# Kernel optimization log

Hardware: AMD Instinct MI355X
Metric: run time of the kernel (lower is better)

The kernel has to match this reference:

```python
import jax, jax.numpy as jnp
import numpy as np

IN_C = 256
INTER_C = 128  # in_channels // reduction_ratio


def setup_inputs() -> dict:
    key = jax.random.key(0)
    ks = jax.random.split(key, 9)
    s = 1.0 / np.sqrt(IN_C)
    si = 1.0 / np.sqrt(INTER_C)
    return {
        "x": jax.random.normal(ks[0], (8, IN_C, 64, 64), dtype=jnp.float32),
        "g_w": jax.random.uniform(ks[1], (INTER_C, IN_C), jnp.float32, -s, s),
        "g_b": jax.random.uniform(ks[2], (INTER_C,), jnp.float32, -s, s),
        "theta_w": jax.random.uniform(ks[3], (INTER_C, IN_C), jnp.float32, -s, s),
        "theta_b": jax.random.uniform(ks[4], (INTER_C,), jnp.float32, -s, s),
        "phi_w": jax.random.uniform(ks[5], (INTER_C, IN_C), jnp.float32, -s, s),
        "phi_b": jax.random.uniform(ks[6], (INTER_C,), jnp.float32, -s, s),
        "W_w": jax.random.uniform(ks[7], (IN_C, INTER_C), jnp.float32, -si, si),
        "W_b": jax.random.uniform(ks[8], (IN_C,), jnp.float32, -si, si),
    }


def _conv1x1(x, w, b):
    # x: [b, cin, h, w]; w: [cout, cin] -> [b, cout, h, w]
    return jnp.einsum('oc,bchw->bohw', w, x) + b[None, :, None, None]


def reference(x, g_w, g_b, theta_w, theta_b, phi_w, phi_b, W_w, W_b):
    b, c, h, w = x.shape
    n = h * w
    g_x = _conv1x1(x, g_w, g_b).reshape(b, INTER_C, n)        # [b, i, n]
    theta_x = _conv1x1(x, theta_w, theta_b).reshape(b, INTER_C, n)
    phi_x = _conv1x1(x, phi_w, phi_b).reshape(b, INTER_C, n)
    # f[b, q, k] = sum_i theta[b, i, q] * phi[b, i, k]
    f = jnp.einsum('biq,bik->bqk', theta_x, phi_x)            # [b, n, n]
    f_div_C = jax.nn.softmax(f, axis=-1)
    # y[b, q, i] = sum_k f_div_C[b, q, k] * g_x[b, i, k]
    y = jnp.einsum('bqk,bik->biq', f_div_C, g_x)              # [b, i, n]
    y = y.reshape(b, INTER_C, h, w)
    W_y = _conv1x1(y, W_w, W_b)
    return W_y + x
```

## Files before the change

### kernel.cpp

```cpp
#include <hip/hip_runtime.h>
#include <hip/hip_bf16.h>
#include <stdint.h>

#define NB 8
#define CIN 256
#define IC 128
#define NP 4096

typedef __attribute__((ext_vector_type(8))) short s8v;
typedef __attribute__((ext_vector_type(4))) short s4v;
typedef __attribute__((ext_vector_type(16))) float f16v;
typedef __attribute__((ext_vector_type(4))) float f4v;

#define MFMA32(a, b, c) __builtin_amdgcn_mfma_f32_32x32x16_bf16(a, b, c, 0, 0, 0)

__device__ __forceinline__ unsigned short f2bf(float f) {
  union { float f; unsigned int u; } v; v.f = f;
  unsigned int u = v.u;
  return (unsigned short)((u + 0x7FFFu + ((u >> 16) & 1u)) >> 16);
}

__device__ __forceinline__ unsigned short f2bf_h(float f) {
  __hip_bfloat16 h = __float2bfloat16(f);
  union { __hip_bfloat16 h; unsigned short u; } cv; cv.h = h;
  return cv.u;
}

__device__ __forceinline__ float bf2f(short s) {
  union { unsigned int u; float f; } cv;
  cv.u = ((unsigned int)(unsigned short)s) << 16;
  return cv.f;
}

typedef const unsigned int __attribute__((address_space(1))) gas_u32;
typedef unsigned int __attribute__((address_space(3))) las_u32;
__device__ __forceinline__ void gload_lds16(const void* g, void* l) {
  __builtin_amdgcn_global_load_lds((gas_u32*)g, (las_u32*)l, 16, 0, 0);
}

__global__ __launch_bounds__(256) void k_wprep(const float* __restrict__ thw,
    const float* __restrict__ phw, const float* __restrict__ gw,
    const float* __restrict__ Ww, unsigned short* __restrict__ wB) {
  const int g = blockIdx.x >> 5;
  const int base = (blockIdx.x & 31) * 1024 + threadIdx.x * 4;
  const float* src = (g == 0) ? thw : ((g == 1) ? phw : ((g == 2) ? gw : Ww));
  const float sc = (g == 0) ? 1.44269504f : 1.0f;
  const f4v v = *(const f4v*)(src + base);
  ushort4 u;
  u.x = f2bf(v[0] * sc); u.y = f2bf(v[1] * sc);
  u.z = f2bf(v[2] * sc); u.w = f2bf(v[3] * sc);
  *(ushort4*)(wB + g * 32768 + base) = u;
}

__global__ __launch_bounds__(256) void k_conv3(const float* __restrict__ x,
    const unsigned short* __restrict__ wB,
    const float* __restrict__ thb, const float* __restrict__ phb,
    const float* __restrict__ gb,
    unsigned short* __restrict__ Qg, unsigned short* __restrict__ Kg,
    unsigned short* __restrict__ Vtg) {
  __shared__ unsigned short X[64 * 256];
  __shared__ unsigned short T[64][72];
  const int t = threadIdx.x, lane = t & 63, wid = t >> 6;
  const int b = blockIdx.x & 7;
  const int p0 = (blockIdx.x >> 3) * 64;
  const int hl = lane >> 5;
  const float* xb = x + (size_t)b * CIN * NP + p0;
  const int cl = t >> 4;
  const int p4 = (t & 15) * 4;
  for (int sub = 0; sub < 4; ++sub) {
    const int c0 = sub * 64;
#pragma unroll
    for (int j = 0; j < 4; ++j) {
      const int cloc = cl + j * 16;
      const f4v v = *(const f4v*)(xb + (size_t)(c0 + cloc) * NP + p4);
      ushort4 u;
      u.x = f2bf(v[0]); u.y = f2bf(v[1]); u.z = f2bf(v[2]); u.w = f2bf(v[3]);
      *(ushort4*)&T[cloc][p4 ^ ((cloc & 7) * 8)] = u;
    }
    __syncthreads();
    const int p = t >> 2;
#pragma unroll
    for (int half = 0; half < 2; ++half) {
      const int cg = (t & 3) + half * 4;
      alignas(16) unsigned short outv[8];
#pragma unroll
      for (int k = 0; k < 8; ++k)
        outv[k] = T[cg * 8 + k][p ^ (k * 8)];
      const int cc = sub * 8 + cg;
      *(uint4*)&X[p * 256 + 8 * (cc ^ (2 * (p & 15)))] = *(const uint4*)outv;
    }
    __syncthreads();
  }
  const int orow = wid * 32 + (lane & 31);

  for (int mat = 0; mat < 3; ++mat) {
    const unsigned short* WB = wB + mat * 32768;
    const float* Bs = (mat == 0) ? thb : ((mat == 1) ? phb : gb);
    const float wsc = (mat == 0) ? 1.44269504f : 1.0f;
    s8v wf[16];
#pragma unroll
    for (int s = 0; s < 16; ++s)
      wf[s] = *(const s8v*)&WB[(size_t)orow * CIN + hl * 8 + 16 * s];
    float br[16];
#pragma unroll
    for (int r = 0; r < 16; ++r)
      br[r] = Bs[wid * 32 + (r & 3) + 8 * (r >> 2) + 4 * hl] * wsc;

#pragma unroll
    for (int nt = 0; nt < 2; ++nt) {
      const int p = (lane & 31) + nt * 32;
      f16v acc;
#pragma unroll
      for (int i = 0; i < 16; ++i) acc[i] = 0.f;
#pragma unroll
      for (int s = 0; s < 16; ++s) {
        const int cc0 = hl + 2 * s;
        const s8v xf = *(const s8v*)&X[p * 256 + 8 * (cc0 ^ (2 * (p & 15)))];
        acc = MFMA32(wf[s], xf, acc);
      }
      if (mat < 2) {
        unsigned short* G = ((mat == 0) ? Qg : Kg) + ((size_t)b * NP + p0 + p) * IC;
#pragma unroll
        for (int grp = 0; grp < 4; ++grp) {
          const int d0 = wid * 32 + 8 * grp + 4 * hl;
          ushort4 u;
          u.x = f2bf(acc[grp * 4 + 0] + br[grp * 4 + 0]);
          u.y = f2bf(acc[grp * 4 + 1] + br[grp * 4 + 1]);
          u.z = f2bf(acc[grp * 4 + 2] + br[grp * 4 + 2]);
          u.w = f2bf(acc[grp * 4 + 3] + br[grp * 4 + 3]);
          *(ushort4*)(G + d0) = u;
        }
      } else {
        unsigned short* G = Vtg + (size_t)b * IC * NP + p0 + p;
#pragma unroll
        for (int r = 0; r < 16; ++r) {
          const int row = wid * 32 + (r & 3) + 8 * (r >> 2) + 4 * hl;
          G[(size_t)row * NP] = f2bf(acc[r] + br[r]);
        }
      }
    }
  }
}

__global__ __launch_bounds__(256, 3) void k_attn(const unsigned short* __restrict__ Qg,
    const unsigned short* __restrict__ Kg, const unsigned short* __restrict__ Vtg,
    unsigned short* __restrict__ Opart, float2* __restrict__ stats) {
  __shared__ unsigned short Klds[2][32 * 128];
  __shared__ unsigned short Vlds[2][128 * 34];
  const int t = threadIdx.x, lane = t & 63, wid = t >> 6;
  const int bid = blockIdx.x;
  const int b = bid & 7;
  const int q0 = ((bid >> 3) & 31) * 128;
  const int half = bid >> 8;
  const int kvbase = half * 2048;
  const int hl = lane >> 5;
  const int q = q0 + wid * 32 + (lane & 31);
  const unsigned short* Qp = Qg + (size_t)b * NP * IC + (size_t)q * IC;
  s8v qf[8];
#pragma unroll
  for (int s = 0; s < 8; ++s)
    qf[s] = *(const s8v*)(Qp + hl * 8 + 16 * s);
  f16v oa[4];
#pragma unroll
  for (int dt = 0; dt < 4; ++dt)
#pragma unroll
    for (int i = 0; i < 16; ++i) oa[dt][i] = 0.f;
  float m = -3.0e38f, lsum = 0.f;
  const unsigned short* Kb = Kg + (size_t)b * NP * IC;
  const unsigned short* Vb = Vtg + (size_t)b * IC * NP;
  const int vd = t >> 2, vc = t & 3;

  uint4 vreg[2];
#pragma unroll
  for (int r = 0; r < 2; ++r) {
    const int ci = wid * 128 + r * 64 + lane;
    const int kv = ci >> 4, cc = ci & 15;
    gload_lds16(Kb + (size_t)(kvbase + kv) * IC + 8 * (cc ^ (kv & 15)),
                (char*)&Klds[0][0] + wid * 2048 + r * 1024);
  }
  {
    const unsigned short* vs = Vb + kvbase + vc * 8;
    vreg[0] = *(const uint4*)(vs + (size_t)vd * NP);
    vreg[1] = *(const uint4*)(vs + (size_t)(vd + 64) * NP);
    *(uint4*)&Vlds[0][vd * 34 + vc * 8] = vreg[0];
    *(uint4*)&Vlds[0][(vd + 64) * 34 + vc * 8] = vreg[1];
  }
  __syncthreads();

  for (int i = 0; i < 64; ++i) {
    const int cur = i & 1;
    const bool more = (i < 63);
    if (more) {
      const int kv0n = kvbase + (i + 1) * 32;
      const unsigned short* vs = Vb + kv0n + vc * 8;
      vreg[0] = *(const uint4*)(vs + (size_t)vd * NP);
      vreg[1] = *(const uint4*)(vs + (size_t)(vd + 64) * NP);
#pragma unroll
      for (int r = 0; r < 2; ++r) {
        const int ci = wid * 128 + r * 64 + lane;
        const int kv = ci >> 4, cc = ci & 15;
        gload_lds16(Kb + (size_t)(kv0n + kv) * IC + 8 * (cc ^ (kv & 15)),
                    (char*)&Klds[cur ^ 1][0] + wid * 2048 + r * 1024);
      }
    }
    f16v sa, sb;
#pragma unroll
    for (int ii = 0; ii < 16; ++ii) { sa[ii] = 0.f; sb[ii] = 0.f; }
    const int kva = lane & 31;
    __builtin_amdgcn_s_setprio(1);
#pragma unroll
    for (int s = 0; s < 8; s += 2) {
      const int cc0 = hl + 2 * s;
      const s8v ka0 = *(const s8v*)&Klds[cur][kva * 128 + 8 * (cc0 ^ (kva & 15))];
      const s8v ka1 = *(const s8v*)&Klds[cur][kva * 128 + 8 * ((cc0 + 2) ^ (kva & 15))];
      sa = MFMA32(ka0, qf[s], sa);
      sb = MFMA32(ka1, qf[s + 1], sb);
    }
    __builtin_amdgcn_s_setprio(0);
    f16v st = sa + sb;
    float tm[8];
#pragma unroll
    for (int ii = 0; ii < 8; ++ii) tm[ii] = fmaxf(st[ii], st[ii + 8]);
#pragma unroll
    for (int w = 4; w >= 1; w >>= 1)
#pragma unroll
      for (int ii = 0; ii < 8; ++ii) if (ii < w) tm[ii] = fmaxf(tm[ii], tm[ii + w]);
    const float pmax = fmaxf(tm[0], __shfl_xor(tm[0], 32));
    if (__any(pmax > m + 8.f)) {
      const float mn = fmaxf(m, pmax);
      const float sc = __builtin_amdgcn_exp2f(m - mn);
      m = mn;
      lsum *= sc;
#pragma unroll
      for (int dt = 0; dt < 4; ++dt)
#pragma unroll
        for (int ii = 0; ii < 16; ++ii) oa[dt][ii] *= sc;
    }
#pragma unroll
    for (int ii = 0; ii < 16; ++ii) st[ii] = __builtin_amdgcn_exp2f(st[ii] - m);
    float ts[8];
#pragma unroll
    for (int ii = 0; ii < 8; ++ii) ts[ii] = st[ii] + st[ii + 8];
#pragma unroll
    for (int w = 4; w >= 1; w >>= 1)
#pragma unroll
      for (int ii = 0; ii < 8; ++ii) if (ii < w) ts[ii] += ts[ii + w];
    lsum += ts[0] + __shfl_xor(ts[0], 32);
    s8v pf0, pf1;
#pragma unroll
    for (int ii = 0; ii < 8; ++ii) {
      pf0[ii] = (short)f2bf_h(st[ii]);
      pf1[ii] = (short)f2bf_h(st[8 + ii]);
    }
    if (more) {
      *(uint4*)&Vlds[cur ^ 1][vd * 34 + vc * 8] = vreg[0];
      *(uint4*)&Vlds[cur ^ 1][(vd + 64) * 34 + vc * 8] = vreg[1];
    }
    __builtin_amdgcn_s_setprio(1);
#pragma unroll
    for (int ks = 0; ks < 2; ++ks) {
      const s8v pcur = (ks == 0) ? pf0 : pf1;
      const int k0 = 16 * ks + 4 * hl;
#pragma unroll
      for (int dt = 0; dt < 4; ++dt) {
        const int d = dt * 32 + (lane & 31);
        const s4v va  = *(const s4v*)&Vlds[cur][d * 34 + k0];
        const s4v vb2 = *(const s4v*)&Vlds[cur][d * 34 + k0 + 8];
        s8v vf;
        vf[0] = va[0]; vf[1] = va[1]; vf[2] = va[2]; vf[3] = va[3];
        vf[4] = vb2[0]; vf[5] = vb2[1]; vf[6] = vb2[2]; vf[7] = vb2[3];
        oa[dt] = MFMA32(vf, pcur, oa[dt]);
      }
    }
    __builtin_amdgcn_s_setprio(0);
    __syncthreads();
  }
  const float inv = 1.0f / lsum;
  unsigned short* Op = Opart + (size_t)half * NB * NP * IC + ((size_t)b * NP + q) * IC;
#pragma unroll
  for (int dt = 0; dt < 4; ++dt) {
#pragma unroll
    for (int grp = 0; grp < 4; ++grp) {
      const int d0 = dt * 32 + 8 * grp + 4 * hl;
      ushort4 u;
      u.x = f2bf_h(oa[dt][grp * 4 + 0] * inv);
      u.y = f2bf_h(oa[dt][grp * 4 + 1] * inv);
      u.z = f2bf_h(oa[dt][grp * 4 + 2] * inv);
      u.w = f2bf_h(oa[dt][grp * 4 + 3] * inv);
      *(ushort4*)(Op + d0) = u;
    }
  }
  if (hl == 0)
    stats[(size_t)half * NB * NP + (size_t)b * NP + q] = make_float2(m, lsum);
}

__global__ __launch_bounds__(256) void k_out(const unsigned short* __restrict__ Opart,
    const float2* __restrict__ stats,
    const unsigned short* __restrict__ WwB, const float* __restrict__ Wb,
    const float* __restrict__ x, float* __restrict__ out) {
  __shared__ unsigned short Y[64 * 128];
  const int t = threadIdx.x, lane = t & 63, wid = t >> 6;
  const int b = blockIdx.x & 7;
  const int p0 = (blockIdx.x >> 3) * 64;
  const int hl = lane >> 5;
  {
    const int p = t >> 2;
    const int quarter = t & 3;
    const int ihb = quarter * 32;
    const int gq = p0 + p;
    const float2 s0 = stats[(size_t)b * NP + gq];
    const float2 s1 = stats[(size_t)NB * NP + (size_t)b * NP + gq];
    const float mm = fmaxf(s0.x, s1.x);
    const float w0 = s0.y * exp2f(s0.x - mm);
    const float w1 = s1.y * exp2f(s1.x - mm);
    const float rinv = 1.0f / (w0 + w1);
    const float a0 = w0 * rinv, a1 = w1 * rinv;
    const unsigned short* P0 = Opart + ((size_t)b * NP + gq) * IC + ihb;
    const unsigned short* P1 = Opart + (size_t)NB * NP * IC + ((size_t)b * NP + gq) * IC + ihb;
#pragma unroll
    for (int c8 = 0; c8 < 4; ++c8) {
      const s8v v0 = *(const s8v*)(P0 + c8 * 8);
      const s8v v1 = *(const s8v*)(P1 + c8 * 8);
      alignas(16) unsigned short o[8];
#pragma unroll
      for (int j = 0; j < 8; ++j)
        o[j] = f2bf_h(a0 * bf2f(v0[j]) + a1 * bf2f(v1[j]));
      const int cc = quarter * 4 + c8;
      *(uint4*)&Y[p * 128 + 8 * (cc ^ (p & 15))] = *(const uint4*)o;
    }
  }
  __syncthreads();
  for (int mt = 0; mt < 2; ++mt) {
    const int orow = mt * 128 + wid * 32 + (lane & 31);
    s8v wf[8];
#pragma unroll
    for (int s = 0; s < 8; ++s)
      wf[s] = *(const s8v*)&WwB[(size_t)orow * IC + hl * 8 + 16 * s];
    float br[16];
#pragma unroll
    for (int r = 0; r < 16; ++r)
      br[r] = Wb[mt * 128 + wid * 32 + (r & 3) + 8 * (r >> 2) + 4 * hl];
#pragma unroll
    for (int nt = 0; nt < 2; ++nt) {
      const int p = (lane & 31) + nt * 32;
      f16v acc;
#pragma unroll
      for (int i = 0; i < 16; ++i) acc[i] = 0.f;
#pragma unroll
      for (int s = 0; s < 8; ++s) {
        const int cc0 = hl + 2 * s;
        const s8v yf = *(const s8v*)&Y[p * 128 + 8 * (cc0 ^ (p & 15))];
        acc = MFMA32(wf[s], yf, acc);
      }
      const size_t pidx = (size_t)b * CIN * NP + (size_t)(p0 + p);
#pragma unroll
      for (int r = 0; r < 16; ++r) {
        const int row = mt * 128 + wid * 32 + (r & 3) + 8 * (r >> 2) + 4 * hl;
        const size_t idx = pidx + (size_t)row * NP;
        out[idx] = acc[r] + br[r] + x[idx];
      }
    }
  }
}

extern "C" void kernel_launch(void* const* d_in, const int* in_sizes, int n_in,
                              void* d_out, int out_size, void* d_ws, size_t ws_size,
                              hipStream_t stream) {
  const float* x   = (const float*)d_in[0];
  const float* gw  = (const float*)d_in[1];
  const float* gb  = (const float*)d_in[2];
  const float* thw = (const float*)d_in[3];
  const float* thb = (const float*)d_in[4];
  const float* phw = (const float*)d_in[5];
  const float* phb = (const float*)d_in[6];
  const float* Ww  = (const float*)d_in[7];
  const float* Wb  = (const float*)d_in[8];
  float* out = (float*)d_out;

  unsigned short* ws  = (unsigned short*)d_ws;
  unsigned short* Opart = ws;
  unsigned short* Qg  = ws + 8388608;
  unsigned short* Kg  = Qg + 4194304;
  unsigned short* Vtg = Kg + 4194304;
  float2* stats = (float2*)(Vtg + 4194304);
  unsigned short* wB = Vtg + 4194304 + 262144;

  k_wprep<<<dim3(128), dim3(256), 0, stream>>>(thw, phw, gw, Ww, wB);
  k_conv3<<<dim3(512), dim3(256), 0, stream>>>(x, wB, thb, phb, gb,
                                               Qg, Kg, Vtg);
  k_attn<<<dim3(512), dim3(256), 0, stream>>>(Qg, Kg, Vtg, Opart, stats);
  k_out<<<dim3(512), dim3(256), 0, stream>>>(Opart, stats, wB + 98304, Wb, x, out);
}
```

Before: 149.4 us.

## Split attention KV range three ways instead of two to raise grid occupancy

The attention kernel now divides the key/value sequence into three chunks (43/43/42 tiles) rather than two halves, launching 768 blocks instead of 512. The output kernel merges three partial results using their max/sum statistics. The aim is to fill more of the GPU's compute units and improve wave balance with launch bounds of 3 blocks per CU. The cost is an extra partial-output buffer write and read plus more merge arithmetic.

```diff
diff --git a/kernel.cpp b/kernel.cpp
--- a/kernel.cpp
+++ b/kernel.cpp
@@ -144,15 +144,17 @@
 
 __global__ __launch_bounds__(256, 3) void k_attn(const unsigned short* __restrict__ Qg,
     const unsigned short* __restrict__ Kg, const unsigned short* __restrict__ Vtg,
-    unsigned short* __restrict__ Opart, float2* __restrict__ stats) {
+    unsigned short* __restrict__ Opart01, unsigned short* __restrict__ Opart2,
+    float2* __restrict__ stats) {
   __shared__ unsigned short Klds[2][32 * 128];
   __shared__ unsigned short Vlds[2][128 * 34];
   const int t = threadIdx.x, lane = t & 63, wid = t >> 6;
   const int bid = blockIdx.x;
   const int b = bid & 7;
   const int q0 = ((bid >> 3) & 31) * 128;
-  const int half = bid >> 8;
-  const int kvbase = half * 2048;
+  const int split = bid >> 8;
+  const int tstart = (split == 0) ? 0 : ((split == 1) ? 43 : 86);
+  const int tend   = (split == 0) ? 43 : ((split == 1) ? 86 : 128);
   const int hl = lane >> 5;
   const int q = q0 + wid * 32 + (lane & 31);
   const unsigned short* Qp = Qg + (size_t)b * NP * IC + (size_t)q * IC;
@@ -175,11 +177,11 @@
   for (int r = 0; r < 2; ++r) {
     const int ci = wid * 128 + r * 64 + lane;
     const int kv = ci >> 4, cc = ci & 15;
-    gload_lds16(Kb + (size_t)(kvbase + kv) * IC + 8 * (cc ^ (kv & 15)),
+    gload_lds16(Kb + (size_t)(tstart * 32 + kv) * IC + 8 * (cc ^ (kv & 15)),
                 (char*)&Klds[0][0] + wid * 2048 + r * 1024);
   }
   {
-    const unsigned short* vs = Vb + kvbase + vc * 8;
+    const unsigned short* vs = Vb + tstart * 32 + vc * 8;
     vreg[0] = *(const uint4*)(vs + (size_t)vd * NP);
     vreg[1] = *(const uint4*)(vs + (size_t)(vd + 64) * NP);
     *(uint4*)&Vlds[0][vd * 34 + vc * 8] = vreg[0];
@@ -187,11 +189,11 @@
   }
   __syncthreads();
 
-  for (int i = 0; i < 64; ++i) {
-    const int cur = i & 1;
-    const bool more = (i < 63);
+  for (int i = tstart; i < tend; ++i) {
+    const int cur = (i - tstart) & 1;
+    const bool more = (i < tend - 1);
     if (more) {
-      const int kv0n = kvbase + (i + 1) * 32;
+      const int kv0n = (i + 1) * 32;
       const unsigned short* vs = Vb + kv0n + vc * 8;
       vreg[0] = *(const uint4*)(vs + (size_t)vd * NP);
       vreg[1] = *(const uint4*)(vs + (size_t)(vd + 64) * NP);
@@ -276,7 +278,9 @@
     __syncthreads();
   }
   const float inv = 1.0f / lsum;
-  unsigned short* Op = Opart + (size_t)half * NB * NP * IC + ((size_t)b * NP + q) * IC;
+  unsigned short* Obase = (split == 2) ? Opart2
+                        : Opart01 + (size_t)split * NB * NP * IC;
+  unsigned short* Op = Obase + ((size_t)b * NP + q) * IC;
 #pragma unroll
   for (int dt = 0; dt < 4; ++dt) {
 #pragma unroll
@@ -291,10 +295,11 @@
     }
   }
   if (hl == 0)
-    stats[(size_t)half * NB * NP + (size_t)b * NP + q] = make_float2(m, lsum);
-}
-
-__global__ __launch_bounds__(256) void k_out(const unsigned short* __restrict__ Opart,
+    stats[(size_t)split * NB * NP + (size_t)b * NP + q] = make_float2(m, lsum);
+}
+
+__global__ __launch_bounds__(256) void k_out(const unsigned short* __restrict__ Opart01,
+    const unsigned short* __restrict__ Opart2,
     const float2* __restrict__ stats,
     const unsigned short* __restrict__ WwB, const float* __restrict__ Wb,
     const float* __restrict__ x, float* __restrict__ out) {
@@ -310,21 +315,26 @@
     const int gq = p0 + p;
     const float2 s0 = stats[(size_t)b * NP + gq];
     const float2 s1 = stats[(size_t)NB * NP + (size_t)b * NP + gq];
-    const float mm = fmaxf(s0.x, s1.x);
+    const float2 s2 = stats[(size_t)2 * NB * NP + (size_t)b * NP + gq];
+    const float mm = fmaxf(fmaxf(s0.x, s1.x), s2.x);
     const float w0 = s0.y * exp2f(s0.x - mm);
     const float w1 = s1.y * exp2f(s1.x - mm);
-    const float rinv = 1.0f / (w0 + w1);
-    const float a0 = w0 * rinv, a1 = w1 * rinv;
-    const unsigned short* P0 = Opart + ((size_t)b * NP + gq) * IC + ihb;
-    const unsigned short* P1 = Opart + (size_t)NB * NP * IC + ((size_t)b * NP + gq) * IC + ihb;
+    const float w2 = s2.y * exp2f(s2.x - mm);
+    const float rinv = 1.0f / (w0 + w1 + w2);
+    const float a0 = w0 * rinv, a1 = w1 * rinv, a2 = w2 * rinv;
+    const size_t rowoff = ((size_t)b * NP + gq) * IC + ihb;
+    const unsigned short* P0 = Opart01 + rowoff;
+    const unsigned short* P1 = Opart01 + (size_t)NB * NP * IC + rowoff;
+    const unsigned short* P2 = Opart2 + rowoff;
 #pragma unroll
     for (int c8 = 0; c8 < 4; ++c8) {
       const s8v v0 = *(const s8v*)(P0 + c8 * 8);
       const s8v v1 = *(const s8v*)(P1 + c8 * 8);
+      const s8v v2 = *(const s8v*)(P2 + c8 * 8);
       alignas(16) unsigned short o[8];
 #pragma unroll
       for (int j = 0; j < 8; ++j)
-        o[j] = f2bf_h(a0 * bf2f(v0[j]) + a1 * bf2f(v1[j]));
+        o[j] = f2bf_h(a0 * bf2f(v0[j]) + a1 * bf2f(v1[j]) + a2 * bf2f(v2[j]));
       const int cc = quarter * 4 + c8;
       *(uint4*)&Y[p * 128 + 8 * (cc ^ (p & 15))] = *(const uint4*)o;
     }
@@ -378,16 +388,18 @@
   float* out = (float*)d_out;
 
   unsigned short* ws  = (unsigned short*)d_ws;
-  unsigned short* Opart = ws;
+  unsigned short* Opart01 = ws;
   unsigned short* Qg  = ws + 8388608;
   unsigned short* Kg  = Qg + 4194304;
   unsigned short* Vtg = Kg + 4194304;
   float2* stats = (float2*)(Vtg + 4194304);
-  unsigned short* wB = Vtg + 4194304 + 262144;
+  unsigned short* wB = Vtg + 4194304 + 393216;
+  unsigned short* Opart2 = wB + 131072;
 
   k_wprep<<<dim3(128), dim3(256), 0, stream>>>(thw, phw, gw, Ww, wB);
   k_conv3<<<dim3(512), dim3(256), 0, stream>>>(x, wB, thb, phb, gb,
                                                Qg, Kg, Vtg);
-  k_attn<<<dim3(512), dim3(256), 0, stream>>>(Qg, Kg, Vtg, Opart, stats);
-  k_out<<<dim3(512), dim3(256), 0, stream>>>(Opart, stats, wB + 98304, Wb, x, out);
-}
+  k_attn<<<dim3(768), dim3(256), 0, stream>>>(Qg, Kg, Vtg, Opart01, Opart2, stats);
+  k_out<<<dim3(512), dim3(256), 0, stream>>>(Opart01, Opart2, stats,
+                                             wB + 98304, Wb, x, out);
+}
```

After: 170.1 us. 1.14x slower.
